# Performance work log

Measured on AMD Instinct MI355X. Metric: run time of the kernel, lower is better.

## Reference

```python
import jax, jax.numpy as jnp
import numpy as np

DIM = 1024
DFF = 4096
LN_EPS = 1e-5


def _layernorm(x, g, b):
    mu = jnp.mean(x, axis=-1, keepdims=True)
    var = jnp.mean((x - mu) ** 2, axis=-1, keepdims=True)
    return (x - mu) * jax.lax.rsqrt(var + LN_EPS) * g + b


def setup_inputs() -> dict:
    key = jax.random.key(0)
    ks = jax.random.split(key, 16)
    B, L, D, F = 4, 2048, DIM, DFF
    return {
        "x": jax.random.normal(ks[0], (B, L, D), dtype=jnp.float32),
        "hidden_real": jax.random.normal(ks[1], (B, D), dtype=jnp.float32),
        "hidden_imag": jax.random.normal(ks[2], (B, D), dtype=jnp.float32),
        # SConvLayer params (real/imag pairs, mirroring torch.view_as_real storage)
        "phazor_init": jax.random.normal(ks[3], (D, 2), dtype=jnp.float32),
        "phazor": jax.random.normal(ks[4], (D, 2), dtype=jnp.float32),
        # fc (gate) linear
        "fc_w": jax.random.normal(ks[5], (D, D), dtype=jnp.float32) / np.sqrt(D),
        "fc_b": jax.random.normal(ks[6], (D,), dtype=jnp.float32) * 0.01,
        # FFN
        "w1": jax.random.normal(ks[7], (F, D), dtype=jnp.float32) / np.sqrt(D),
        "b1": jax.random.normal(ks[8], (F,), dtype=jnp.float32) * 0.01,
        "w2": jax.random.normal(ks[9], (D, F), dtype=jnp.float32) / np.sqrt(F),
        "b2": jax.random.normal(ks[10], (D,), dtype=jnp.float32) * 0.01,
        # shared LayerNorm (used twice in the block with the same params)
        "ln_g": jnp.ones((D,), dtype=jnp.float32),
        "ln_b": jnp.zeros((D,), dtype=jnp.float32),
    }


def reference(x, hidden_real, hidden_imag, phazor_init, phazor,
              fc_w, fc_b, w1, b1, w2, b2, ln_g, ln_b):
    B, L, D = x.shape
    hidden = (hidden_real + 1j * hidden_imag).astype(jnp.complex64)

    x_res = x
    xn = _layernorm(x, ln_g, ln_b)

    # --- SConvLayer ---
    pz = (phazor[:, 0] + 1j * phazor[:, 1]).astype(jnp.complex64)  # [D]
    # magnitude exp(-|z|^2), phase = angle(z)
    p = jnp.exp(-(pz.real ** 2 + pz.imag ** 2)) * jnp.exp(1j * jnp.angle(pz))
    t = jnp.arange(L)
    prog = p[None, :] ** t[:, None]                      # [L, D] complex
    init_c = (phazor_init[:, 0] + 1j * phazor_init[:, 1]).astype(jnp.complex64)
    filt = prog * init_c[None, :]                        # [L, D]
    n2 = 2 * L
    filt_fft = jnp.fft.fft(filt, n=n2, axis=0)           # [2L, D]
    x_fft = jnp.fft.fft(xn.astype(jnp.complex64), n=n2, axis=1)  # [B, 2L, D]
    conv = jnp.fft.ifft(filt_fft[None] * x_fft, axis=1)[:, :L]   # [B, L, D]
    conv_with_past = conv + hidden[:, None, :] * prog[None] * p[None, None, :]
    sx = conv_with_past.real

    # --- gate ---
    y = jax.nn.silu(jnp.einsum('bld,ed->ble', x_res, fc_w) + fc_b)
    x2 = sx * y + x_res

    # --- FFN (same LayerNorm params) ---
    x3 = _layernorm(x2, ln_g, ln_b)
    h = jax.nn.silu(jnp.einsum('bld,fd->blf', x3, w1) + b1)
    out = jnp.einsum('blf,df->bld', h, w2) + b2 + x2
    return out, conv_with_past
```

## Files before the change

kernel.cpp:

```cpp
#include <hip/hip_runtime.h>
#include <hip/hip_bf16.h>

#define D_MODEL 1024
#define D_FF    4096
#define SEQ_LEN 2048
#define NBATCH  4
#define NROWS   (NBATCH*SEQ_LEN)
#define NCHUNK  32
#define CHUNK_L (SEQ_LEN/NCHUNK)
#define LN_EPS  1e-5f

typedef __hip_bfloat16 bf16;
typedef __attribute__((ext_vector_type(8))) short bf16x8;
typedef __attribute__((ext_vector_type(4))) float f32x4;

__device__ __forceinline__ void gload16(const bf16* g, bf16* l) {
    __builtin_amdgcn_global_load_lds(
        (const __attribute__((address_space(1))) void*)g,
        (__attribute__((address_space(3))) void*)l, 16, 0, 0);
}

__global__ void cast4(const float4* __restrict__ in, ushort4* __restrict__ out, int n4) {
    int i = blockIdx.x * blockDim.x + threadIdx.x;
    if (i < n4) {
        float4 v = in[i];
        union { ushort4 u; bf16 b[4]; } cv;
        cv.b[0] = __float2bfloat16(v.x); cv.b[1] = __float2bfloat16(v.y);
        cv.b[2] = __float2bfloat16(v.z); cv.b[3] = __float2bfloat16(v.w);
        out[i] = cv.u;
    }
}

__global__ void compute_pvec(const float* __restrict__ phz, float* __restrict__ pv) {
    int d = blockIdx.x * blockDim.x + threadIdx.x;
    if (d >= D_MODEL) return;
    float re = phz[2*d], im = phz[2*d+1];
    float r2 = re*re + im*im;
    float mag = expf(-r2);
    float pr, pim;
    if (r2 > 0.f) { float inv = mag / sqrtf(r2); pr = re*inv; pim = im*inv; }
    else          { pr = mag; pim = 0.f; }
    float ar = pr, ai = pim;
    #pragma unroll
    for (int i = 0; i < 6; i++) { float nr = ar*ar - ai*ai; float ni = 2.f*ar*ai; ar = nr; ai = ni; }
    pv[d]            = pr;
    pv[D_MODEL+d]    = pim;
    pv[2*D_MODEL+d]  = ar;
    pv[3*D_MODEL+d]  = ai;
}

__global__ __launch_bounds__(256) void ln_fused(const float* __restrict__ x,
                                                const float* __restrict__ g,
                                                const float* __restrict__ bta,
                                                float* __restrict__ outf,
                                                bf16*  __restrict__ outb,
                                                bf16*  __restrict__ rawb)
{
    int row = blockIdx.x;
    int tid = threadIdx.x;
    const float4* xr = (const float4*)(x + (size_t)row * D_MODEL);
    float4 v = xr[tid];
    if (rawb) {
        union { ushort4 u; bf16 b[4]; } cv;
        cv.b[0]=__float2bfloat16(v.x); cv.b[1]=__float2bfloat16(v.y);
        cv.b[2]=__float2bfloat16(v.z); cv.b[3]=__float2bfloat16(v.w);
        ((ushort4*)(rawb + (size_t)row * D_MODEL))[tid] = cv.u;
    }
    float s  = v.x + v.y + v.z + v.w;
    float s2 = v.x*v.x + v.y*v.y + v.z*v.z + v.w*v.w;
    for (int off = 32; off; off >>= 1) { s += __shfl_down(s, off); s2 += __shfl_down(s2, off); }
    __shared__ float red[8];
    int wid = tid >> 6, lane = tid & 63;
    if (lane == 0) { red[wid] = s; red[4+wid] = s2; }
    __syncthreads();
    if (tid == 0) {
        red[0] = red[0]+red[1]+red[2]+red[3];
        red[4] = red[4]+red[5]+red[6]+red[7];
    }
    __syncthreads();
    float mu  = red[0] * (1.f/D_MODEL);
    float var = red[4] * (1.f/D_MODEL) - mu*mu;
    float rstd = rsqrtf(var + LN_EPS);
    float4 gv = ((const float4*)g)[tid];
    float4 bv = ((const float4*)bta)[tid];
    float4 o;
    o.x = (v.x-mu)*rstd*gv.x + bv.x;
    o.y = (v.y-mu)*rstd*gv.y + bv.y;
    o.z = (v.z-mu)*rstd*gv.z + bv.z;
    o.w = (v.w-mu)*rstd*gv.w + bv.w;
    if (outf) ((float4*)(outf + (size_t)row * D_MODEL))[tid] = o;
    if (outb) {
        union { ushort4 u; bf16 b[4]; } cv;
        cv.b[0]=__float2bfloat16(o.x); cv.b[1]=__float2bfloat16(o.y);
        cv.b[2]=__float2bfloat16(o.z); cv.b[3]=__float2bfloat16(o.w);
        ((ushort4*)(outb + (size_t)row * D_MODEL))[tid] = cv.u;
    }
}

__global__ __launch_bounds__(256) void gate_ln(const float* __restrict__ cwp, int cstride,
                                               const bf16*  __restrict__ y,
                                               const float* __restrict__ x,
                                               const float* __restrict__ g,
                                               const float* __restrict__ bta,
                                               float* __restrict__ x2,
                                               bf16*  __restrict__ x3b)
{
    int row = blockIdx.x;
    int tid = threadIdx.x;
    size_t base = (size_t)row * D_MODEL + tid*4;
    float4 xv = *(const float4*)(x + base);
    union { ushort4 u; bf16 b[4]; } yv;
    yv.u = *(const ushort4*)(y + base);
    float4 cw;
    if (cstride == 1) {
        cw = *(const float4*)(cwp + base);
    } else {
        const float2* cp = (const float2*)cwp + base;
        cw.x = cp[0].x; cw.y = cp[1].x; cw.z = cp[2].x; cw.w = cp[3].x;
    }
    float4 v;
    v.x = cw.x * __bfloat162float(yv.b[0]) + xv.x;
    v.y = cw.y * __bfloat162float(yv.b[1]) + xv.y;
    v.z = cw.z * __bfloat162float(yv.b[2]) + xv.z;
    v.w = cw.w * __bfloat162float(yv.b[3]) + xv.w;
    *(float4*)(x2 + base) = v;

    float s  = v.x + v.y + v.z + v.w;
    float s2 = v.x*v.x + v.y*v.y + v.z*v.z + v.w*v.w;
    for (int off = 32; off; off >>= 1) { s += __shfl_down(s, off); s2 += __shfl_down(s2, off); }
    __shared__ float red[8];
    int wid = tid >> 6, lane = tid & 63;
    if (lane == 0) { red[wid] = s; red[4+wid] = s2; }
    __syncthreads();
    if (tid == 0) {
        red[0] = red[0]+red[1]+red[2]+red[3];
        red[4] = red[4]+red[5]+red[6]+red[7];
    }
    __syncthreads();
    float mu  = red[0] * (1.f/D_MODEL);
    float var = red[4] * (1.f/D_MODEL) - mu*mu;
    float rstd = rsqrtf(var + LN_EPS);
    float4 gv = ((const float4*)g)[tid];
    float4 bv = ((const float4*)bta)[tid];
    union { ushort4 u; bf16 b[4]; } cv;
    cv.b[0] = __float2bfloat16((v.x-mu)*rstd*gv.x + bv.x);
    cv.b[1] = __float2bfloat16((v.y-mu)*rstd*gv.y + bv.y);
    cv.b[2] = __float2bfloat16((v.z-mu)*rstd*gv.z + bv.z);
    cv.b[3] = __float2bfloat16((v.w-mu)*rstd*gv.w + bv.w);
    *(ushort4*)(x3b + base) = cv.u;
}

__global__ __launch_bounds__(256) void scan_pass1(const float* __restrict__ xn,
                                                  const float* __restrict__ pv,
                                                  const float* __restrict__ pini,
                                                  float* __restrict__ Sc)
{
    int d = blockIdx.x * 256 + threadIdx.x;
    int c = blockIdx.y, b = blockIdx.z;
    float pr = pv[d], pim = pv[D_MODEL+d];
    float icr = pini[2*d], ici = pini[2*d+1];
    float Sr = 0.f, Si = 0.f;
    const float* xp = xn + ((size_t)b*SEQ_LEN + c*CHUNK_L) * D_MODEL + d;
    #pragma unroll 8
    for (int i = 0; i < CHUNK_L; i++) {
        float xv = xp[(size_t)i * D_MODEL];
        float nr = pr*Sr - pim*Si + icr*xv;
        float ni = pr*Si + pim*Sr + ici*xv;
        Sr = nr; Si = ni;
    }
    size_t o = ((size_t)b*NCHUNK + c) * D_MODEL + d;
    Sc[2*o] = Sr; Sc[2*o+1] = Si;
}

__global__ __launch_bounds__(256) void scan_prefix(const float* __restrict__ Sc,
                                                   const float* __restrict__ pv,
                                                   const float* __restrict__ hr,
                                                   const float* __restrict__ hi,
                                                   float* __restrict__ pref)
{
    int d = blockIdx.x * 256 + threadIdx.x;
    int b = blockIdx.y;
    float qr = pv[2*D_MODEL+d], qi = pv[3*D_MODEL+d];
    float Ur = hr[b*D_MODEL+d], Ui = hi[b*D_MODEL+d];
    for (int c = 0; c < NCHUNK; c++) {
        size_t o = ((size_t)b*NCHUNK + c) * D_MODEL + d;
        pref[2*o] = Ur; pref[2*o+1] = Ui;
        float sr = Sc[2*o], si = Sc[2*o+1];
        float nr = qr*Ur - qi*Ui + sr;
        float ni = qr*Ui + qi*Ur + si;
        Ur = nr; Ui = ni;
    }
}

__global__ __launch_bounds__(256) void scan_pass2(const float* __restrict__ xn,
                                                  const float* __restrict__ pv,
                                                  const float* __restrict__ pini,
                                                  const float* __restrict__ pref,
                                                  float* __restrict__ cwp,
                                                  int interleaved)
{
    int d = blockIdx.x * 256 + threadIdx.x;
    int c = blockIdx.y, b = blockIdx.z;
    float pr = pv[d], pim = pv[D_MODEL+d];
    float icr = pini[2*d], ici = pini[2*d+1];
    size_t po = ((size_t)b*NCHUNK + c) * D_MODEL + d;
    float Ur = pref[2*po], Ui = pref[2*po+1];
    size_t base = ((size_t)b*SEQ_LEN + c*CHUNK_L) * D_MODEL + d;
    const float* xp = xn + base;
    if (interleaved) {
        float2* cp = (float2*)cwp + base;
        #pragma unroll 8
        for (int i = 0; i < CHUNK_L; i++) {
            float xv = xp[(size_t)i * D_MODEL];
            float nr = pr*Ur - pim*Ui + icr*xv;
            float ni = pr*Ui + pim*Ur + ici*xv;
            Ur = nr; Ui = ni;
            cp[(size_t)i * D_MODEL] = make_float2(Ur, Ui);
        }
    } else {
        float* cp = cwp + base;
        #pragma unroll 8
        for (int i = 0; i < CHUNK_L; i++) {
            float xv = xp[(size_t)i * D_MODEL];
            float nr = pr*Ur - pim*Ui + icr*xv;
            float ni = pr*Ui + pim*Ur + ici*xv;
            Ur = nr; Ui = ni;
            cp[(size_t)i * D_MODEL] = Ur;
        }
    }
}

template<int EPI>
__device__ __forceinline__ void epi_store(float v, size_t idx,
                                          const float* e0, int e0_stride, const float* e1,
                                          float* outf, bf16* outb)
{
    if (EPI == 1) {
        float yv = v / (1.f + __expf(-v));
        outb[idx] = __float2bfloat16(yv);
    } else {
        outf[idx] = v + e0[idx];
    }
}

#define BM 128
#define BN 128
#define BK 32

template<int EPI>
__global__ __launch_bounds__(256) void gemm_bt(const bf16* __restrict__ A,
                                               const bf16* __restrict__ Bt,
                                               const float* __restrict__ bias,
                                               const float* __restrict__ e0, int e0_stride,
                                               const float* __restrict__ e1,
                                               float* __restrict__ outf,
                                               bf16*  __restrict__ outb,
                                               int M, int N, int K)
{
    __shared__ __align__(16) bf16 As[3][BM*BK];
    __shared__ __align__(16) bf16 Bs[3][BM*BK];
    int tid = threadIdx.x;
    int m0 = blockIdx.x * BM;
    int n0 = blockIdx.y * BN;

    int wid = tid >> 6, lane = tid & 63;
    int wm = (wid >> 1) * 64, wn = (wid & 1) * 64;
    int lr = lane & 15;
    int lkc = lane >> 4;

    int rl = lane >> 2;
    int cS = (lane & 3) ^ ((rl >> 1) & 3);
    const bf16* gA0 = A  + (size_t)(m0 +      wid*16 + rl) * K + cS*8;
    const bf16* gA1 = A  + (size_t)(m0 + 64 + wid*16 + rl) * K + cS*8;
    const bf16* gB0 = Bt + (size_t)(n0 +      wid*16 + rl) * K + cS*8;
    const bf16* gB1 = Bt + (size_t)(n0 + 64 + wid*16 + rl) * K + cS*8;
    int lo0 = (     wid*16) * BK;
    int lo1 = (64 + wid*16) * BK;

    int keyr = (lr >> 1) & 3;
    int cR = (lkc ^ keyr) * 8;
    int offA[4], offB[4];
    #pragma unroll
    for (int i = 0; i < 4; i++) {
        offA[i] = (wm + i*16 + lr) * BK + cR;
        offB[i] = (wn + i*16 + lr) * BK + cR;
    }

    int nt = K / BK;
    auto stage = [&](int slot, int tile) {
        int k0 = tile * BK;
        gload16(gA0 + k0, &As[slot][lo0]);
        gload16(gA1 + k0, &As[slot][lo1]);
        gload16(gB0 + k0, &Bs[slot][lo0]);
        gload16(gB1 + k0, &Bs[slot][lo1]);
    };
    f32x4 acc[4][4] = {};
    auto compute = [&](int slot) {
        bf16x8 af[4], bfv[4];
        #pragma unroll
        for (int i = 0; i < 4; i++) {
            af[i]  = *(const bf16x8*)&As[slot][offA[i]];
            bfv[i] = *(const bf16x8*)&Bs[slot][offB[i]];
        }
        #pragma unroll
        for (int i = 0; i < 4; i++)
            #pragma unroll
            for (int j = 0; j < 4; j++)
                acc[i][j] = __builtin_amdgcn_mfma_f32_16x16x32_bf16(af[i], bfv[j], acc[i][j], 0, 0, 0);
    };

    stage(0, 0); stage(1, 1); stage(2, 2);

    int s = 0;
    for (int t = 0; t < nt - 3; ++t) {
        asm volatile("s_waitcnt vmcnt(8)" ::: "memory");
        __builtin_amdgcn_s_barrier();
        __builtin_amdgcn_sched_barrier(0);
        compute(s);
        asm volatile("" ::: "memory");
        __builtin_amdgcn_s_barrier();
        stage(s, t + 3);
        s = (s == 2) ? 0 : s + 1;
    }
    asm volatile("s_waitcnt vmcnt(8)" ::: "memory");
    __builtin_amdgcn_s_barrier();
    __builtin_amdgcn_sched_barrier(0);
    compute(s);
    s = (s == 2) ? 0 : s + 1;
    asm volatile("s_waitcnt vmcnt(4)" ::: "memory");
    __builtin_amdgcn_s_barrier();
    __builtin_amdgcn_sched_barrier(0);
    compute(s);
    s = (s == 2) ? 0 : s + 1;
    asm volatile("s_waitcnt vmcnt(0)" ::: "memory");
    __builtin_amdgcn_s_barrier();
    __builtin_amdgcn_sched_barrier(0);
    compute(s);

    int mrow = 4 * (lane >> 4);
    #pragma unroll
    for (int i = 0; i < 4; i++) {
        #pragma unroll
        for (int j = 0; j < 4; j++) {
            int nb = n0 + wn + j*16 + lr;
            float bb = bias[nb];
            #pragma unroll
            for (int r = 0; r < 4; r++) {
                int m = m0 + wm + i*16 + mrow + r;
                size_t idx = (size_t)m * N + nb;
                epi_store<EPI>(acc[i][j][r] + bb, idx, e0, e0_stride, e1, outf, outb);
            }
        }
    }
}

#define TM 256
#define TN 256

template<int EPI>
__global__ __launch_bounds__(512, 2) void gemm256p(const bf16* __restrict__ A,
                                                   const bf16* __restrict__ Bt,
                                                   const float* __restrict__ bias,
                                                   const float* __restrict__ e0, int e0_stride,
                                                   const float* __restrict__ e1,
                                                   float* __restrict__ outf,
                                                   bf16*  __restrict__ outb,
                                                   int M, int N, int K)
{
    __shared__ __align__(16) bf16 As[3][TM*BK];
    __shared__ __align__(16) bf16 Bs[3][TN*BK];
    int tid = threadIdx.x;
    int m0 = blockIdx.x * TM;
    int n0 = blockIdx.y * TN;

    int wid = tid >> 6, lane = tid & 63;
    int wr = wid >> 2, wc = wid & 3;
    int wm = wr * 128, wn = wc * 64;
    int lr = lane & 15;
    int lkc = lane >> 4;

    int rs = tid >> 2;
    int cS = (tid & 3) ^ ((rs >> 1) & 3);
    const bf16* gA = A  + (size_t)m0 * K + cS*8;
    const bf16* gB = Bt + (size_t)n0 * K + cS*8;
    int ldst = tid * 8;

    int keyr = (lr >> 1) & 3;
    int cR = (lkc ^ keyr) * 8;
    int offA[8], offB[4];
    #pragma unroll
    for (int i = 0; i < 8; i++) offA[i] = (wm + i*16 + lr) * BK + cR;
    #pragma unroll
    for (int j = 0; j < 4; j++) offB[j] = (wn + j*16 + lr) * BK + cR;

    int nt = K / BK;
    auto stA = [&](int slot, int tile) {
        int k0 = tile * BK;
        gload16(gA + (size_t)rs * K + k0,         &As[slot][ldst]);
        gload16(gA + (size_t)(128 + rs) * K + k0, &As[slot][4096 + ldst]);
    };
    auto stB = [&](int slot, int tile) {
        int k0 = tile * BK;
        gload16(gB + (size_t)rs * K + k0,         &Bs[slot][ldst]);
        gload16(gB + (size_t)(128 + rs) * K + k0, &Bs[slot][4096 + ldst]);
    };

    f32x4 acc[8][4] = {};
    stA(0, 0); stB(0, 0); stA(1, 1); stB(1, 1); stB(2, 2);

    int s = 0;
    for (int t = 0; t < nt; ++t) {
        int sA = (s >= 1) ? s - 1 : 2;
        if (t < nt - 2)       { asm volatile("s_waitcnt vmcnt(6)" ::: "memory"); }
        else if (t == nt - 2) { asm volatile("s_waitcnt vmcnt(4)" ::: "memory"); }
        else                  { asm volatile("s_waitcnt vmcnt(0)" ::: "memory"); }
        __builtin_amdgcn_s_barrier();
        asm volatile("" ::: "memory");
        bf16x8 af0[4], bfv[4];
        #pragma unroll
        for (int i = 0; i < 4; i++) af0[i] = *(const bf16x8*)&As[s][offA[i]];
        #pragma unroll
        for (int j = 0; j < 4; j++) bfv[j] = *(const bf16x8*)&Bs[s][offB[j]];
        if (t + 2 < nt) stA(sA, t + 2);
        asm volatile("s_waitcnt lgkmcnt(0)" ::: "memory");
        __builtin_amdgcn_sched_barrier(0);
        __builtin_amdgcn_s_setprio(1);
        #pragma unroll
        for (int i = 0; i < 4; i++)
            #pragma unroll
            for (int j = 0; j < 4; j++)
                acc[i][j] = __builtin_amdgcn_mfma_f32_16x16x32_bf16(af0[i], bfv[j], acc[i][j], 0, 0, 0);
        __builtin_amdgcn_s_setprio(0);
        __builtin_amdgcn_s_barrier();
        asm volatile("" ::: "memory");
        bf16x8 af1[4];
        #pragma unroll
        for (int i = 0; i < 4; i++) af1[i] = *(const bf16x8*)&As[s][offA[4+i]];
        if (t + 3 < nt) stB(s, t + 3);
        asm volatile("s_waitcnt lgkmcnt(0)" ::: "memory");
        __builtin_amdgcn_sched_barrier(0);
        __builtin_amdgcn_s_setprio(1);
        #pragma unroll
        for (int i = 0; i < 4; i++)
            #pragma unroll
            for (int j = 0; j < 4; j++)
                acc[4+i][j] = __builtin_amdgcn_mfma_f32_16x16x32_bf16(af1[i], bfv[j], acc[4+i][j], 0, 0, 0);
        __builtin_amdgcn_s_setprio(0);
        s = (s == 2) ? 0 : s + 1;
    }
    asm volatile("s_waitcnt vmcnt(0)" ::: "memory");

    int mrow = 4 * (lane >> 4);
    #pragma unroll
    for (int i = 0; i < 8; i++) {
        #pragma unroll
        for (int j = 0; j < 4; j++) {
            int nb = n0 + wn + j*16 + lr;
            float bb = bias[nb];
            #pragma unroll
            for (int r = 0; r < 4; r++) {
                int m = m0 + wm + i*16 + mrow + r;
                size_t idx = (size_t)m * N + nb;
                epi_store<EPI>(acc[i][j][r] + bb, idx, e0, e0_stride, e1, outf, outb);
            }
        }
    }
}

extern "C" void kernel_launch(void* const* d_in, const int* in_sizes, int n_in,
                              void* d_out, int out_size, void* d_ws, size_t ws_size,
                              hipStream_t stream)
{
    const float* x    = (const float*)d_in[0];
    const float* hr   = (const float*)d_in[1];
    const float* hi   = (const float*)d_in[2];
    const float* pini = (const float*)d_in[3];
    const float* phz  = (const float*)d_in[4];
    const float* fcw  = (const float*)d_in[5];
    const float* fcb  = (const float*)d_in[6];
    const float* w1   = (const float*)d_in[7];
    const float* b1   = (const float*)d_in[8];
    const float* w2   = (const float*)d_in[9];
    const float* b2   = (const float*)d_in[10];
    const float* lng  = (const float*)d_in[11];
    const float* lnb  = (const float*)d_in[12];

    float* out = (float*)d_out;
    float* cwp = out + (size_t)NROWS * D_MODEL;
    int interleaved = (out_size >= NROWS * D_MODEL * 3) ? 1 : 0;

    char* ws = (char*)d_ws;
    size_t off = 0;
    bf16*  wfcb = (bf16*)(ws + off);  off += (size_t)D_MODEL*D_MODEL*2;
    bf16*  w1b  = (bf16*)(ws + off);  off += (size_t)D_FF*D_MODEL*2;
    bf16*  w2b  = (bf16*)(ws + off);  off += (size_t)D_MODEL*D_FF*2;
    float* pv   = (float*)(ws + off); off += (size_t)4*D_MODEL*4;
    float* xn   = (float*)(ws + off); off += (size_t)NROWS*D_MODEL*4;
    bf16*  xbf  = (bf16*)(ws + off);  off += (size_t)NROWS*D_MODEL*2;
    float* Sc   = (float*)(ws + off); off += (size_t)NBATCH*NCHUNK*D_MODEL*2*4;
    float* pref = (float*)(ws + off); off += (size_t)NBATCH*NCHUNK*D_MODEL*2*4;
    float* x2   = (float*)(ws + off); off += (size_t)NROWS*D_MODEL*4;
    bf16*  x3b  = (bf16*)(ws + off);  off += (size_t)NROWS*D_MODEL*2;
    bf16*  hbuf = (bf16*)(ws + off);  off += (size_t)NROWS*D_FF*2;
    bf16*  ybuf = (bf16*)(ws + off);  off += (size_t)NROWS*D_MODEL*2;

    cast4<<<1024, 256, 0, stream>>>((const float4*)fcw, (ushort4*)wfcb, D_MODEL*D_MODEL/4);
    cast4<<<4096, 256, 0, stream>>>((const float4*)w1,  (ushort4*)w1b,  D_FF*D_MODEL/4);
    cast4<<<4096, 256, 0, stream>>>((const float4*)w2,  (ushort4*)w2b,  D_MODEL*D_FF/4);

    compute_pvec<<<4, 256, 0, stream>>>(phz, pv);

    ln_fused<<<NROWS, 256, 0, stream>>>(x, lng, lnb, xn, nullptr, xbf);

    scan_pass1<<<dim3(4, NCHUNK, NBATCH), 256, 0, stream>>>(xn, pv, pini, Sc);
    scan_prefix<<<dim3(4, NBATCH), 256, 0, stream>>>(Sc, pv, hr, hi, pref);
    scan_pass2<<<dim3(4, NCHUNK, NBATCH), 256, 0, stream>>>(xn, pv, pini, pref, cwp, interleaved);

    gemm_bt<1><<<dim3(NROWS/BM, D_MODEL/BN), 256, 0, stream>>>(
        xbf, wfcb, fcb, nullptr, 1, nullptr, nullptr, ybuf, NROWS, D_MODEL, D_MODEL);

    gate_ln<<<NROWS, 256, 0, stream>>>(cwp, interleaved ? 2 : 1, ybuf, x, lng, lnb, x2, x3b);

    gemm256p<1><<<dim3(NROWS/TM, D_FF/TN), 512, 0, stream>>>(
        x3b, w1b, b1, nullptr, 1, nullptr, nullptr, hbuf, NROWS, D_FF, D_MODEL);

    gemm_bt<2><<<dim3(NROWS/BM, D_MODEL/BN), 256, 0, stream>>>(
        hbuf, w2b, b2, x2, 1, nullptr, out, nullptr, NROWS, D_MODEL, D_FF);
}
```

Before: 280.7 us.

## Split GEMM main loop into two half-phases with staggered A/B prefetch

Restructures the 3-slot GEMM pipeline so each K-tile is computed in two halves of 8 MFMAs each. The A and B tile loads are issued separately: A is prefetched two tiles ahead into the previously consumed slot, and B three tiles ahead after the first half finishes reading it. s_setprio raises wave priority around the MFMA bursts. The aim is finer-grained overlap of global-to-LDS loads with MFMA work, at the cost of more barriers per tile and a more fragile slot/waitcnt accounting.

After: 284.3 us. Within noise of the previous version (+1.3%).

```diff
diff --git a/kernel.cpp b/kernel.cpp
--- a/kernel.cpp
+++ b/kernel.cpp
@@ -287,55 +287,61 @@
     }
 
     int nt = K / BK;
-    auto stage = [&](int slot, int tile) {
+    auto stA = [&](int slot, int tile) {
         int k0 = tile * BK;
         gload16(gA0 + k0, &As[slot][lo0]);
         gload16(gA1 + k0, &As[slot][lo1]);
+    };
+    auto stB = [&](int slot, int tile) {
+        int k0 = tile * BK;
         gload16(gB0 + k0, &Bs[slot][lo0]);
         gload16(gB1 + k0, &Bs[slot][lo1]);
     };
+
     f32x4 acc[4][4] = {};
-    auto compute = [&](int slot) {
-        bf16x8 af[4], bfv[4];
-        #pragma unroll
-        for (int i = 0; i < 4; i++) {
-            af[i]  = *(const bf16x8*)&As[slot][offA[i]];
-            bfv[i] = *(const bf16x8*)&Bs[slot][offB[i]];
-        }
-        #pragma unroll
-        for (int i = 0; i < 4; i++)
+    stA(0, 0); stB(0, 0); stA(1, 1); stB(1, 1); stB(2, 2);
+
+    int s = 0;
+    for (int t = 0; t < nt; ++t) {
+        int sA = (s >= 1) ? s - 1 : 2;
+        if (t < nt - 2)       { asm volatile("s_waitcnt vmcnt(6)" ::: "memory"); }
+        else if (t == nt - 2) { asm volatile("s_waitcnt vmcnt(4)" ::: "memory"); }
+        else                  { asm volatile("s_waitcnt vmcnt(0)" ::: "memory"); }
+        __builtin_amdgcn_s_barrier();
+        asm volatile("" ::: "memory");
+        bf16x8 af0[2], bfv[4];
+        #pragma unroll
+        for (int i = 0; i < 2; i++) af0[i] = *(const bf16x8*)&As[s][offA[i]];
+        #pragma unroll
+        for (int j = 0; j < 4; j++) bfv[j] = *(const bf16x8*)&Bs[s][offB[j]];
+        if (t + 2 < nt) stA(sA, t + 2);
+        asm volatile("s_waitcnt lgkmcnt(0)" ::: "memory");
+        __builtin_amdgcn_sched_barrier(0);
+        __builtin_amdgcn_s_setprio(1);
+        #pragma unroll
+        for (int i = 0; i < 2; i++)
             #pragma unroll
             for (int j = 0; j < 4; j++)
-                acc[i][j] = __builtin_amdgcn_mfma_f32_16x16x32_bf16(af[i], bfv[j], acc[i][j], 0, 0, 0);
-    };
-
-    stage(0, 0); stage(1, 1); stage(2, 2);
-
-    int s = 0;
-    for (int t = 0; t < nt - 3; ++t) {
-        asm volatile("s_waitcnt vmcnt(8)" ::: "memory");
+                acc[i][j] = __builtin_amdgcn_mfma_f32_16x16x32_bf16(af0[i], bfv[j], acc[i][j], 0, 0, 0);
+        __builtin_amdgcn_s_setprio(0);
         __builtin_amdgcn_s_barrier();
+        asm volatile("" ::: "memory");
+        bf16x8 af1[2];
+        #pragma unroll
+        for (int i = 0; i < 2; i++) af1[i] = *(const bf16x8*)&As[s][offA[2+i]];
+        if (t + 3 < nt) stB(s, t + 3);
+        asm volatile("s_waitcnt lgkmcnt(0)" ::: "memory");
         __builtin_amdgcn_sched_barrier(0);
-        compute(s);
-        asm volatile("" ::: "memory");
-        __builtin_amdgcn_s_barrier();
-        stage(s, t + 3);
+        __builtin_amdgcn_s_setprio(1);
+        #pragma unroll
+        for (int i = 0; i < 2; i++)
+            #pragma unroll
+            for (int j = 0; j < 4; j++)
+                acc[2+i][j] = __builtin_amdgcn_mfma_f32_16x16x32_bf16(af1[i], bfv[j], acc[2+i][j], 0, 0, 0);
+        __builtin_amdgcn_s_setprio(0);
         s = (s == 2) ? 0 : s + 1;
     }
-    asm volatile("s_waitcnt vmcnt(8)" ::: "memory");
-    __builtin_amdgcn_s_barrier();
-    __builtin_amdgcn_sched_barrier(0);
-    compute(s);
-    s = (s == 2) ? 0 : s + 1;
-    asm volatile("s_waitcnt vmcnt(4)" ::: "memory");
-    __builtin_amdgcn_s_barrier();
-    __builtin_amdgcn_sched_barrier(0);
-    compute(s);
-    s = (s == 2) ? 0 : s + 1;
     asm volatile("s_waitcnt vmcnt(0)" ::: "memory");
-    __builtin_amdgcn_s_barrier();
-    __builtin_amdgcn_sched_barrier(0);
-    compute(s);
 
     int mrow = 4 * (lane >> 4);
     #pragma unroll
```
